# Kernel optimization log

Hardware: AMD Instinct MI355X
Metric: run time of the kernel (lower is better)

Reference implementation:

```python
import jax, jax.numpy as jnp
import numpy as np

B, L, E, H, D = 4, 4096, 1024, 16, 64  # batch, seq, embed, heads, head_dim
EPS = 1e-6


def setup_inputs() -> dict:
    key = jax.random.key(0)
    k1, k2, k3 = jax.random.split(key, 3)
    return {
        "q": jax.random.normal(k1, (B, L, E), dtype=jnp.float32),
        "k": jax.random.normal(k2, (B, L, E), dtype=jnp.float32),
        "v": jax.random.normal(k3, (B, L, E), dtype=jnp.float32),
        "mask": jnp.ones((B, L), dtype=jnp.float32),
    }


def _split_heads(x):
    # (B, L, E) -> (B*H, L, D)
    return x.reshape(B, L, H, D).transpose(0, 2, 1, 3).reshape(B * H, L, D)


def reference(q, k, v, mask):
    # feature map: relu
    q = jax.nn.relu(q)
    k = jax.nn.relu(k)
    # padding mask applied to keys/values
    k = k * mask[:, :, None]
    v = v * mask[:, :, None]
    q = _split_heads(q)
    k = _split_heads(k)
    v = _split_heads(v)
    # cosFormer sin/cos reweighting: pi/2 * i / m for i = 1..L
    idx = (np.pi / 2) * jnp.arange(1, L + 1, dtype=jnp.float32) / L
    s = jnp.sin(idx)[None, :, None]  # (1, L, 1)
    c = jnp.cos(idx)[None, :, None]
    q_ = jnp.concatenate([q * s, q * c], axis=-1)  # (B*H, L, 2D)
    k_ = jnp.concatenate([k * s, k * c], axis=-1)
    # linear-attention KV accumulation (non-causal): (B*H, 2D, D)
    kv = jnp.einsum('nld,nlm->ndm', k_, v)
    # normalizer
    z = 1.0 / jnp.maximum(jnp.einsum('nld,nd->nl', q_, k_.sum(axis=1)), EPS)
    out = jnp.einsum('nld,ndm,nl->nlm', q_, kv, z)  # (B*H, L, D)
    return out.reshape(B, H, L, D)
```

## Files before the change

### kernel.cpp

```cpp
#include <hip/hip_runtime.h>
#include <hip/hip_bf16.h>
#include <math.h>

#define B_ 4
#define L_ 4096
#define E_ 1024
#define H_ 16
#define D_ 64
#define N_ 64
#define D2_ 128
#define EPS_ 1e-6f

#define CH_ 16
#define LC_ (L_ / CH_)
#define ST_ 16
#define NSTG_ 16

#define DANG_ 3.83495197e-4f

typedef short short8 __attribute__((ext_vector_type(8)));
typedef float f32x4 __attribute__((ext_vector_type(4)));
typedef unsigned int u32;
typedef unsigned short u16;

static __device__ __forceinline__ u32 pack2bf(float a, float b) {
  union { __hip_bfloat16 h; u16 s; } x, y;
  x.h = __float2bfloat16(a);
  y.h = __float2bfloat16(b);
  return (u32)x.s | ((u32)y.s << 16);
}

static __device__ __forceinline__ short bf1(float a) {
  union { __hip_bfloat16 h; short s; } x;
  x.h = __float2bfloat16(a);
  return x.s;
}

static __device__ __forceinline__ void gld16(const void* g, void* l) {
  __builtin_amdgcn_global_load_lds(
      (const __attribute__((address_space(1))) unsigned int*)g,
      (__attribute__((address_space(3))) unsigned int*)l, 16, 0, 0);
}

#define BAR_() __builtin_amdgcn_s_barrier()
#define WAIT_LGKM0_()                                     \
  {                                                       \
    asm volatile("s_waitcnt lgkmcnt(0)" ::: "memory");    \
    __builtin_amdgcn_sched_barrier(0);                    \
  }
#define WAIT_VM4_()                                       \
  {                                                       \
    asm volatile("s_waitcnt vmcnt(4)" ::: "memory");      \
    __builtin_amdgcn_sched_barrier(0);                    \
  }
#define WAIT_VM0_()                                       \
  {                                                       \
    asm volatile("s_waitcnt vmcnt(0)" ::: "memory");      \
    __builtin_amdgcn_sched_barrier(0);                    \
  }

__global__ __launch_bounds__(256, 2) void phase1_mfma(
    const float* __restrict__ k, const float* __restrict__ v,
    const float* __restrict__ mask,
    float* __restrict__ part_kv, float* __restrict__ part_ks) {
  __shared__ __align__(16) float kraw[3][ST_ * 128];
  __shared__ __align__(16) float vraw[3][ST_ * 128];
  __shared__ __align__(16) u16 ka[2][D2_ * 36];
  __shared__ __align__(16) u16 vt[2][D_ * 36];
  __shared__ float msh[LC_];

  const int bid = blockIdx.x;
  const int p = bid & 31;
  const int ch = bid >> 5;
  const int b = p >> 3;
  const int hcol0 = (p & 7) * 128;
  const int t = threadIdx.x;
  const int wv = t >> 6;
  const int lane = t & 63;
  const int c_lo = lane & 15;
  const int lp = lane >> 4;
  const int l0 = ch * LC_;

  const int hh = t >> 7;
  const int tt = t & 127;
  const int lp2h = tt >> 4;
  const int dg = tt & 15;

  u32* ka32 = (u32*)ka;
  u32* vt32 = (u32*)vt;

  f32x4 acc[2][2][4];
#pragma unroll
  for (int hq = 0; hq < 2; ++hq)
#pragma unroll
    for (int i = 0; i < 2; ++i)
#pragma unroll
      for (int j = 0; j < 4; ++j) acc[hq][i][j] = (f32x4)0.f;
  f32x4 acc5[2][2];
#pragma unroll
  for (int hq = 0; hq < 2; ++hq) {
    acc5[hq][0] = (f32x4)0.f;
    acc5[hq][1] = (f32x4)0.f;
  }

  short8 bones = {0, 0, 0, 0, 0, 0, 0, 0};
  if (c_lo == 0) {
#pragma unroll
    for (int j = 0; j < 8; ++j) bones[j] = (short)0x3F80;
  }

#define P1_GLD(S, BUF)                                                       \
  do {                                                                       \
    _Pragma("unroll") for (int j_ = 0; j_ < 2; ++j_) {                       \
      const int jr_ = 4 * wv + 2 * j_;                                       \
      const int r_ = jr_ + (lane >> 5);                                      \
      const int g_ = lane & 31;                                              \
      const size_t gs_ = (size_t)(b * L_ + l0 + (S) * ST_ + r_) * E_ +       \
                         hcol0 + ((g_ ^ r_) << 2);                           \
      gld16(k + gs_, &kraw[BUF][jr_ * 128]);                                 \
      gld16(v + gs_, &vraw[BUF][jr_ * 128]);                                 \
    }                                                                        \
  } while (0)

#define P1_PACK(S, BUF)                                                      \
  do {                                                                       \
    const int la_ = 2 * lp2h, lb_ = la_ + 1;                                 \
    const float m0_ = msh[(S) * ST_ + la_];                                  \
    const float m1_ = msh[(S) * ST_ + lb_];                                  \
    const int lga_ = l0 + (S) * ST_ + la_;                                   \
    float s0_, c0_, s1_, c1_;                                                \
    __sincosf((float)(lga_ + 1) * DANG_, &s0_, &c0_);                        \
    __sincosf((float)(lga_ + 2) * DANG_, &s1_, &c1_);                        \
    const int li_ = ((S) & 1) * 8 + lp2h;                                    \
    _Pragma("unroll") for (int dj_ = 0; dj_ < 4; ++dj_) {                    \
      const int d_ = dg + 16 * dj_;                                          \
      const int c_ = hh * 64 + d_;                                           \
      const int G_ = c_ >> 2, su_ = c_ & 3;                                  \
      const float k0_ = kraw[BUF][la_ * 128 + ((G_ ^ la_) << 2) + su_];      \
      const float k1_ = kraw[BUF][lb_ * 128 + ((G_ ^ lb_) << 2) + su_];      \
      const float v0_ = vraw[BUF][la_ * 128 + ((G_ ^ la_) << 2) + su_];      \
      const float v1_ = vraw[BUF][lb_ * 128 + ((G_ ^ lb_) << 2) + su_];      \
      const float kr0_ = fmaxf(k0_, 0.f) * m0_;                              \
      const float kr1_ = fmaxf(k1_, 0.f) * m1_;                              \
      ka32[hh * (D2_ * 18) + d_ * 18 + li_] = pack2bf(kr0_ * s0_, kr1_ * s1_); \
      ka32[hh * (D2_ * 18) + (d_ + 64) * 18 + li_] =                         \
          pack2bf(kr0_ * c0_, kr1_ * c1_);                                   \
      vt32[hh * (D_ * 18) + d_ * 18 + li_] = pack2bf(v0_ * m0_, v1_ * m1_);  \
    }                                                                        \
  } while (0)

#define P1_MMA()                                                             \
  do {                                                                       \
    _Pragma("unroll") for (int hq_ = 0; hq_ < 2; ++hq_) {                    \
      short8 af_[2], bf_[4];                                                 \
      _Pragma("unroll") for (int dt_ = 0; dt_ < 2; ++dt_)                    \
          af_[dt_] = *(const short8*)&ka[hq_][(wv * 32 + dt_ * 16 + c_lo) *  \
                                                 36 + lp * 8];               \
      _Pragma("unroll") for (int mt_ = 0; mt_ < 4; ++mt_)                    \
          bf_[mt_] = *(const short8*)&vt[hq_][(mt_ * 16 + c_lo) * 36 +       \
                                              lp * 8];                       \
      _Pragma("unroll") for (int dt_ = 0; dt_ < 2; ++dt_) {                  \
        _Pragma("unroll") for (int mt_ = 0; mt_ < 4; ++mt_)                  \
            acc[hq_][dt_][mt_] = __builtin_amdgcn_mfma_f32_16x16x32_bf16(    \
                af_[dt_], bf_[mt_], acc[hq_][dt_][mt_], 0, 0, 0);            \
        acc5[hq_][dt_] = __builtin_amdgcn_mfma_f32_16x16x32_bf16(            \
            af_[dt_], bones, acc5[hq_][dt_], 0, 0, 0);                       \
      }                                                                      \
    }                                                                        \
  } while (0)

#define P1_GROUP(S, I3, I4, VMN)                                             \
  do {                                                                       \
    P1_PACK((S), (S) % 3);                                                   \
    BAR_();                           \
    if (I3) P1_GLD((S) + 3, (S) % 3);                                        \
    P1_PACK((S) + 1, ((S) + 1) % 3);                                         \
    WAIT_LGKM0_();                                                           \
    BAR_();                                              \
    if (I4) P1_GLD((S) + 4, ((S) + 1) % 3);                                  \
    P1_MMA();                                                                \
    if ((VMN) == 4) { WAIT_VM4_(); }                                         \
    else if ((VMN) == 0) { WAIT_VM0_(); }                                    \
    BAR_();                             \
  } while (0)

  if (wv == 0) gld16(mask + (size_t)b * L_ + l0 + lane * 4, msh);
  P1_GLD(0, 0);
  P1_GLD(1, 1);
  P1_GLD(2, 2);
  WAIT_VM4_();
  BAR_();

  P1_GROUP(0, 1, 1, 4);
  P1_GROUP(2, 1, 1, 4);
  P1_GROUP(4, 1, 1, 4);
  P1_GROUP(6, 1, 1, 4);
  P1_GROUP(8, 1, 1, 4);
  P1_GROUP(10, 1, 1, 4);
  P1_GROUP(12, 1, 0, 0);
  P1_GROUP(14, 0, 0, -1);

#pragma unroll
  for (int hq = 0; hq < 2; ++hq) {
    const int n = 2 * p + hq;
    const size_t pbase = (size_t)(ch * N_ + n) * (D2_ * D_);
#pragma unroll
    for (int dt = 0; dt < 2; ++dt) {
      const int d = wv * 32 + dt * 16 + lp * 4;
#pragma unroll
      for (int mt = 0; mt < 4; ++mt) {
        const int mcol = mt * 16 + c_lo;
#pragma unroll
        for (int r = 0; r < 4; ++r)
          part_kv[pbase + (size_t)(d + r) * D_ + mcol] = acc[hq][dt][mt][r];
      }
    }
    if (c_lo == 0) {
#pragma unroll
      for (int dt = 0; dt < 2; ++dt)
#pragma unroll
        for (int r = 0; r < 4; ++r)
          part_ks[(size_t)(ch * N_ + n) * D2_ + wv * 32 + dt * 16 + lp * 4 +
                  r] = acc5[hq][dt][r];
    }
  }
}

__global__ __launch_bounds__(256) void reduce_t(
    const float* __restrict__ part_kv, const float* __restrict__ part_ks,
    u16* __restrict__ kvt, float* __restrict__ ks) {
  __shared__ __align__(16) float tsh[16 * 68];
  const int bid = blockIdx.x;
  const int n = bid >> 3;
  const int sl = bid & 7;
  const int t = threadIdx.x;

  const int e0 = sl * 1024 + t * 4;
  f32x4 s = (f32x4)0.f;
#pragma unroll
  for (int cc = 0; cc < CH_; ++cc)
    s += *(const f32x4*)&part_kv[(size_t)(cc * N_ + n) * (D2_ * D_) + e0];
  *(f32x4*)&tsh[(t >> 4) * 68 + (t & 15) * 4] = s;

  if (sl == 0 && t < D2_) {
    float ss = 0.f;
#pragma unroll
    for (int cc = 0; cc < CH_; ++cc)
      ss += part_ks[(size_t)(cc * N_ + n) * D2_ + t];
    ks[n * D2_ + t] = ss;
  }
  __syncthreads();

  const int m = t >> 2;
  const int d4 = (t & 3) * 4;
  const u32 lo = pack2bf(tsh[(d4 + 0) * 68 + m], tsh[(d4 + 1) * 68 + m]);
  const u32 hi = pack2bf(tsh[(d4 + 2) * 68 + m], tsh[(d4 + 3) * 68 + m]);
  uint2 pk; pk.x = lo; pk.y = hi;
  *(uint2*)&kvt[(size_t)n * (D2_ * D_) + (size_t)m * D2_ + sl * 16 + d4] = pk;
}

__global__ __launch_bounds__(256, 3) void phase2_mfma(
    const float* __restrict__ q, const u16* __restrict__ kvt,
    const float* __restrict__ ks, float* __restrict__ out) {
  __shared__ __align__(16) float qsh[2 * 64 * 64];
  __shared__ __align__(16) u16 kbsh[64 * 128];

  const int bid = blockIdx.x;
  const int n = bid & 63;
  const int g2 = bid >> 6;
  const int b = n >> 4, h = n & 15;
  const int t = threadIdx.x;
  const int wv = t >> 6, lane = t & 63;
  const int c_lo = lane & 15, quad = lane >> 4;
  const int l0 = g2 * 128;

  const float* qbase = q + (size_t)(b * L_ + l0) * E_ + h * 64;
  const u16* kvbase = kvt + (size_t)n * (D2_ * D_);
  const int rsub = lane >> 4;
  const int g = lane & 15;
#pragma unroll
  for (int j = 0; j < 4; ++j) {
    const int r = wv * 16 + j * 4 + rsub;
    const int sw = (g ^ (r & 15));
    gld16(kvbase + (size_t)r * D2_ + (sw << 3),
          kbsh + (wv * 16 + j * 4) * 128);
    gld16(qbase + (size_t)r * E_ + (sw << 2),
          qsh + (wv * 16 + j * 4) * 64);
    gld16(qbase + (size_t)(64 + r) * E_ + (sw << 2),
          qsh + 4096 + (wv * 16 + j * 4) * 64);
  }

  const float* ksn = ks + n * D2_;
  short8 bks[4];
#pragma unroll
  for (int kk = 0; kk < 4; ++kk) {
    const f32x4 ka_ = *(const f32x4*)(ksn + kk * 32 + quad * 8);
    const f32x4 kb_ = *(const f32x4*)(ksn + kk * 32 + quad * 8 + 4);
    short8 tt = {0, 0, 0, 0, 0, 0, 0, 0};
    if (c_lo == 0) {
#pragma unroll
      for (int j = 0; j < 4; ++j) {
        tt[j] = bf1(ka_[j]);
        tt[j + 4] = bf1(kb_[j]);
      }
    }
    bks[kk] = tt;
  }

  __syncthreads();

#pragma unroll
  for (int cc = 0; cc < 2; ++cc) {
    const int row = wv * 16 + c_lo;
    const int glr = l0 + cc * 64 + row;
    float sv, cv;
    __sincosf((float)(glr + 1) * DANG_, &sv, &cv);

    const float* qrow = qsh + cc * 4096 + row * 64;
    const int sw = row & 15;
    const f32x4 a0 = *(const f32x4*)(qrow + (((2 * quad) ^ sw) << 2));
    const f32x4 a1 = *(const f32x4*)(qrow + (((2 * quad + 1) ^ sw) << 2));
    const f32x4 a2 = *(const f32x4*)(qrow + (((8 + 2 * quad) ^ sw) << 2));
    const f32x4 a3 = *(const f32x4*)(qrow + (((9 + 2 * quad) ^ sw) << 2));

    short8 af[4];
#pragma unroll
    for (int j = 0; j < 4; ++j) {
      const float x0 = fmaxf(a0[j], 0.f);
      const float x1 = fmaxf(a1[j], 0.f);
      const float x2 = fmaxf(a2[j], 0.f);
      const float x3 = fmaxf(a3[j], 0.f);
      af[0][j] = bf1(x0 * sv); af[0][j + 4] = bf1(x1 * sv);
      af[1][j] = bf1(x2 * sv); af[1][j + 4] = bf1(x3 * sv);
      af[2][j] = bf1(x0 * cv); af[2][j + 4] = bf1(x1 * cv);
      af[3][j] = bf1(x2 * cv); af[3][j + 4] = bf1(x3 * cv);
    }

    f32x4 acc[4];
#pragma unroll
    for (int mt = 0; mt < 4; ++mt) acc[mt] = (f32x4)0.f;
    f32x4 acc5 = (f32x4)0.f;

#pragma unroll
    for (int kk = 0; kk < 4; ++kk) {
#pragma unroll
      for (int mt = 0; mt < 4; ++mt) {
        const int m = mt * 16 + c_lo;
        const short8 bfr = *(const short8*)
            &kbsh[m * 128 + (((kk * 4 + quad) ^ (m & 15)) << 3)];
        acc[mt] =
            __builtin_amdgcn_mfma_f32_16x16x32_bf16(af[kk], bfr, acc[mt], 0, 0, 0);
      }
      acc5 = __builtin_amdgcn_mfma_f32_16x16x32_bf16(af[kk], bks[kk], acc5, 0, 0, 0);
    }

#pragma unroll
    for (int r = 0; r < 4; ++r) {
      const float den = __shfl(acc5[r], quad * 16);
      const float z = 1.f / fmaxf(den, EPS_);
      const int gl = l0 + cc * 64 + wv * 16 + quad * 4 + r;
      const size_t ob = (size_t)n * (L_ * D_) + (size_t)gl * D_;
#pragma unroll
      for (int mt = 0; mt < 4; ++mt)
        out[ob + mt * 16 + c_lo] = acc[mt][r] * z;
    }
  }
}

extern "C" void kernel_launch(void* const* d_in, const int* in_sizes, int n_in,
                              void* d_out, int out_size, void* d_ws,
                              size_t ws_size, hipStream_t stream) {
  const float* q = (const float*)d_in[0];
  const float* k = (const float*)d_in[1];
  const float* v = (const float*)d_in[2];
  const float* mask = (const float*)d_in[3];
  float* out = (float*)d_out;

  float* part_kv = (float*)d_ws;
  float* part_ks = part_kv + (size_t)CH_ * N_ * D2_ * D_;
  u16* kvt = (u16*)(part_ks + (size_t)CH_ * N_ * D2_);
  float* ks = (float*)(kvt + (size_t)N_ * D2_ * D_);

  phase1_mfma<<<dim3(CH_ * 32), dim3(256), 0, stream>>>(k, v, mask, part_kv, part_ks);
  reduce_t<<<dim3(N_ * 8), dim3(256), 0, stream>>>(part_kv, part_ks, kvt, ks);
  phase2_mfma<<<dim3(N_ * 32), dim3(256), 0, stream>>>(q, kvt, ks, out);
}
```

Before: 238.9 us.

## Widen phase1 blocks to 512 threads covering four heads with double buffering

The K/V accumulation kernel now runs 512-thread blocks. Each block handles 256 embedding columns (four heads) per sequence chunk instead of 128, so there are half as many blocks. Each wave pair computes one head's 128x64 KV tile, split across the two waves by d-half. The staging pipeline moves from triple to double buffering of raw global loads, with wait placement adjusted to match. The aim is wider, more coalesced row loads and lower per-block overhead. In exchange the grid shrinks to 256 blocks, LDS use per block rises, and there is less load prefetch depth, which may reduce occupancy and latency hiding.

```diff
diff --git a/kernel.cpp b/kernel.cpp
--- a/kernel.cpp
+++ b/kernel.cpp
@@ -59,27 +59,30 @@
     __builtin_amdgcn_sched_barrier(0);                    \
   }
 
-__global__ __launch_bounds__(256, 2) void phase1_mfma(
+__global__ __launch_bounds__(512, 2) void phase1_mfma(
     const float* __restrict__ k, const float* __restrict__ v,
     const float* __restrict__ mask,
     float* __restrict__ part_kv, float* __restrict__ part_ks) {
-  __shared__ __align__(16) float kraw[3][ST_ * 128];
-  __shared__ __align__(16) float vraw[3][ST_ * 128];
-  __shared__ __align__(16) u16 ka[2][D2_ * 36];
-  __shared__ __align__(16) u16 vt[2][D_ * 36];
+  __shared__ __align__(16) float kraw[2][ST_ * 256];
+  __shared__ __align__(16) float vraw[2][ST_ * 256];
+  __shared__ __align__(16) u16 ka[4 * D2_ * 36];
+  __shared__ __align__(16) u16 vt[4 * D_ * 36];
   __shared__ float msh[LC_];
 
   const int bid = blockIdx.x;
-  const int p = bid & 31;
-  const int ch = bid >> 5;
-  const int b = p >> 3;
-  const int hcol0 = (p & 7) * 128;
+  const int p = bid & 15;
+  const int ch = bid >> 4;
+  const int b = p >> 2;
+  const int hcol0 = (p & 3) * 256;
   const int t = threadIdx.x;
   const int wv = t >> 6;
   const int lane = t & 63;
   const int c_lo = lane & 15;
-  const int lp = lane >> 4;
+  const int lp = (lane >> 4) & 3;
   const int l0 = ch * LC_;
+
+  const int hq = wv >> 1;
+  const int dh = wv & 1;
 
   const int hh = t >> 7;
   const int tt = t & 127;
@@ -89,19 +92,14 @@
   u32* ka32 = (u32*)ka;
   u32* vt32 = (u32*)vt;
 
-  f32x4 acc[2][2][4];
-#pragma unroll
-  for (int hq = 0; hq < 2; ++hq)
-#pragma unroll
-    for (int i = 0; i < 2; ++i)
-#pragma unroll
-      for (int j = 0; j < 4; ++j) acc[hq][i][j] = (f32x4)0.f;
-  f32x4 acc5[2][2];
-#pragma unroll
-  for (int hq = 0; hq < 2; ++hq) {
-    acc5[hq][0] = (f32x4)0.f;
-    acc5[hq][1] = (f32x4)0.f;
-  }
+  f32x4 acc[4][4];
+#pragma unroll
+  for (int i = 0; i < 4; ++i)
+#pragma unroll
+    for (int j = 0; j < 4; ++j) acc[i][j] = (f32x4)0.f;
+  f32x4 acc5[4];
+#pragma unroll
+  for (int i = 0; i < 4; ++i) acc5[i] = (f32x4)0.f;
 
   short8 bones = {0, 0, 0, 0, 0, 0, 0, 0};
   if (c_lo == 0) {
@@ -112,13 +110,11 @@
 #define P1_GLD(S, BUF)                                                       \
   do {                                                                       \
     _Pragma("unroll") for (int j_ = 0; j_ < 2; ++j_) {                       \
-      const int jr_ = 4 * wv + 2 * j_;                                       \
-      const int r_ = jr_ + (lane >> 5);                                      \
-      const int g_ = lane & 31;                                              \
+      const int r_ = 2 * wv + j_;                                            \
       const size_t gs_ = (size_t)(b * L_ + l0 + (S) * ST_ + r_) * E_ +       \
-                         hcol0 + ((g_ ^ r_) << 2);                           \
-      gld16(k + gs_, &kraw[BUF][jr_ * 128]);                                 \
-      gld16(v + gs_, &vraw[BUF][jr_ * 128]);                                 \
+                         hcol0 + ((lane ^ r_) << 2);                         \
+      gld16(k + gs_, &kraw[BUF][r_ * 256]);                                  \
+      gld16(v + gs_, &vraw[BUF][r_ * 256]);                                  \
     }                                                                        \
   } while (0)
 
@@ -136,58 +132,57 @@
       const int d_ = dg + 16 * dj_;                                          \
       const int c_ = hh * 64 + d_;                                           \
       const int G_ = c_ >> 2, su_ = c_ & 3;                                  \
-      const float k0_ = kraw[BUF][la_ * 128 + ((G_ ^ la_) << 2) + su_];      \
-      const float k1_ = kraw[BUF][lb_ * 128 + ((G_ ^ lb_) << 2) + su_];      \
-      const float v0_ = vraw[BUF][la_ * 128 + ((G_ ^ la_) << 2) + su_];      \
-      const float v1_ = vraw[BUF][lb_ * 128 + ((G_ ^ lb_) << 2) + su_];      \
+      const float k0_ = kraw[BUF][la_ * 256 + ((G_ ^ la_) << 2) + su_];      \
+      const float k1_ = kraw[BUF][lb_ * 256 + ((G_ ^ lb_) << 2) + su_];      \
+      const float v0_ = vraw[BUF][la_ * 256 + ((G_ ^ la_) << 2) + su_];      \
+      const float v1_ = vraw[BUF][lb_ * 256 + ((G_ ^ lb_) << 2) + su_];      \
       const float kr0_ = fmaxf(k0_, 0.f) * m0_;                              \
       const float kr1_ = fmaxf(k1_, 0.f) * m1_;                              \
-      ka32[hh * (D2_ * 18) + d_ * 18 + li_] = pack2bf(kr0_ * s0_, kr1_ * s1_); \
-      ka32[hh * (D2_ * 18) + (d_ + 64) * 18 + li_] =                         \
+      ka32[hh * 2304 + d_ * 18 + li_] = pack2bf(kr0_ * s0_, kr1_ * s1_);     \
+      ka32[hh * 2304 + (d_ + 64) * 18 + li_] =                               \
           pack2bf(kr0_ * c0_, kr1_ * c1_);                                   \
-      vt32[hh * (D_ * 18) + d_ * 18 + li_] = pack2bf(v0_ * m0_, v1_ * m1_);  \
+      vt32[hh * 1152 + d_ * 18 + li_] = pack2bf(v0_ * m0_, v1_ * m1_);       \
     }                                                                        \
   } while (0)
 
 #define P1_MMA()                                                             \
   do {                                                                       \
-    _Pragma("unroll") for (int hq_ = 0; hq_ < 2; ++hq_) {                    \
-      short8 af_[2], bf_[4];                                                 \
-      _Pragma("unroll") for (int dt_ = 0; dt_ < 2; ++dt_)                    \
-          af_[dt_] = *(const short8*)&ka[hq_][(wv * 32 + dt_ * 16 + c_lo) *  \
-                                                 36 + lp * 8];               \
+    short8 af_[4], bf_[4];                                                   \
+    _Pragma("unroll") for (int dt_ = 0; dt_ < 4; ++dt_)                      \
+        af_[dt_] = *(const short8*)                                          \
+            &ka[hq * 4608 + (dh * 64 + dt_ * 16 + c_lo) * 36 + lp * 8];      \
+    _Pragma("unroll") for (int mt_ = 0; mt_ < 4; ++mt_)                      \
+        bf_[mt_] = *(const short8*)                                          \
+            &vt[hq * 2304 + (mt_ * 16 + c_lo) * 36 + lp * 8];                \
+    _Pragma("unroll") for (int dt_ = 0; dt_ < 4; ++dt_) {                    \
       _Pragma("unroll") for (int mt_ = 0; mt_ < 4; ++mt_)                    \
-          bf_[mt_] = *(const short8*)&vt[hq_][(mt_ * 16 + c_lo) * 36 +       \
-                                              lp * 8];                       \
-      _Pragma("unroll") for (int dt_ = 0; dt_ < 2; ++dt_) {                  \
-        _Pragma("unroll") for (int mt_ = 0; mt_ < 4; ++mt_)                  \
-            acc[hq_][dt_][mt_] = __builtin_amdgcn_mfma_f32_16x16x32_bf16(    \
-                af_[dt_], bf_[mt_], acc[hq_][dt_][mt_], 0, 0, 0);            \
-        acc5[hq_][dt_] = __builtin_amdgcn_mfma_f32_16x16x32_bf16(            \
-            af_[dt_], bones, acc5[hq_][dt_], 0, 0, 0);                       \
-      }                                                                      \
+          acc[dt_][mt_] = __builtin_amdgcn_mfma_f32_16x16x32_bf16(           \
+              af_[dt_], bf_[mt_], acc[dt_][mt_], 0, 0, 0);                   \
+      acc5[dt_] = __builtin_amdgcn_mfma_f32_16x16x32_bf16(af_[dt_], bones,   \
+                                                          acc5[dt_], 0, 0,   \
+                                                          0);                \
     }                                                                        \
   } while (0)
 
-#define P1_GROUP(S, I3, I4, VMN)                                             \
+#define P1_GROUP(S, MID, END, VMID)                                          \
   do {                                                                       \
-    P1_PACK((S), (S) % 3);                                                   \
-    BAR_();                           \
-    if (I3) P1_GLD((S) + 3, (S) % 3);                                        \
-    P1_PACK((S) + 1, ((S) + 1) % 3);                                         \
+    P1_PACK((S), (S) % 2);                                                   \
+    BAR_();                             \
+    if (MID) P1_GLD((S) + 2, (S) % 2);                                       \
+    if ((VMID) == 4) { WAIT_VM4_(); }                                        \
+    else { WAIT_VM0_(); }                                                    \
+    P1_PACK((S) + 1, ((S) + 1) % 2);                                         \
     WAIT_LGKM0_();                                                           \
     BAR_();                                              \
-    if (I4) P1_GLD((S) + 4, ((S) + 1) % 3);                                  \
+    if (END) P1_GLD((S) + 3, ((S) + 1) % 2);                                 \
     P1_MMA();                                                                \
-    if ((VMN) == 4) { WAIT_VM4_(); }                                         \
-    else if ((VMN) == 0) { WAIT_VM0_(); }                                    \
+    if (END) { WAIT_VM4_(); }                                                \
     BAR_();                             \
   } while (0)
 
   if (wv == 0) gld16(mask + (size_t)b * L_ + l0 + lane * 4, msh);
   P1_GLD(0, 0);
   P1_GLD(1, 1);
-  P1_GLD(2, 2);
   WAIT_VM4_();
   BAR_();
 
@@ -197,32 +192,29 @@
   P1_GROUP(6, 1, 1, 4);
   P1_GROUP(8, 1, 1, 4);
   P1_GROUP(10, 1, 1, 4);
-  P1_GROUP(12, 1, 0, 0);
-  P1_GROUP(14, 0, 0, -1);
-
-#pragma unroll
-  for (int hq = 0; hq < 2; ++hq) {
-    const int n = 2 * p + hq;
-    const size_t pbase = (size_t)(ch * N_ + n) * (D2_ * D_);
-#pragma unroll
-    for (int dt = 0; dt < 2; ++dt) {
-      const int d = wv * 32 + dt * 16 + lp * 4;
-#pragma unroll
-      for (int mt = 0; mt < 4; ++mt) {
-        const int mcol = mt * 16 + c_lo;
-#pragma unroll
-        for (int r = 0; r < 4; ++r)
-          part_kv[pbase + (size_t)(d + r) * D_ + mcol] = acc[hq][dt][mt][r];
-      }
-    }
-    if (c_lo == 0) {
-#pragma unroll
-      for (int dt = 0; dt < 2; ++dt)
-#pragma unroll
-        for (int r = 0; r < 4; ++r)
-          part_ks[(size_t)(ch * N_ + n) * D2_ + wv * 32 + dt * 16 + lp * 4 +
-                  r] = acc5[hq][dt][r];
-    }
+  P1_GROUP(12, 1, 1, 4);
+  P1_GROUP(14, 0, 0, 0);
+
+  const int n = 4 * p + hq;
+  const size_t pbase = (size_t)(ch * N_ + n) * (D2_ * D_);
+#pragma unroll
+  for (int dt = 0; dt < 4; ++dt) {
+    const int d = dh * 64 + dt * 16 + lp * 4;
+#pragma unroll
+    for (int mt = 0; mt < 4; ++mt) {
+      const int mcol = mt * 16 + c_lo;
+#pragma unroll
+      for (int r = 0; r < 4; ++r)
+        part_kv[pbase + (size_t)(d + r) * D_ + mcol] = acc[dt][mt][r];
+    }
+  }
+  if (c_lo == 0) {
+#pragma unroll
+    for (int dt = 0; dt < 4; ++dt)
+#pragma unroll
+      for (int r = 0; r < 4; ++r)
+        part_ks[(size_t)(ch * N_ + n) * D2_ + dh * 64 + dt * 16 + lp * 4 + r] =
+            acc5[dt][r];
   }
 }
 
@@ -381,7 +373,7 @@
   u16* kvt = (u16*)(part_ks + (size_t)CH_ * N_ * D2_);
   float* ks = (float*)(kvt + (size_t)N_ * D2_ * D_);
 
-  phase1_mfma<<<dim3(CH_ * 32), dim3(256), 0, stream>>>(k, v, mask, part_kv, part_ks);
+  phase1_mfma<<<dim3(CH_ * 16), dim3(512), 0, stream>>>(k, v, mask, part_kv, part_ks);
   reduce_t<<<dim3(N_ * 8), dim3(256), 0, stream>>>(part_kv, part_ks, kvt, ks);
   phase2_mfma<<<dim3(N_ * 32), dim3(256), 0, stream>>>(q, kvt, ks, out);
 }
```

Measured after the change: 242.9 us. Within noise of the previous version (+1.7%).
